# Kernel tuning notes

Measured on AMD Instinct MI355X. Metric: run time of the kernel, lower is better.

Reference implementation:

```python
import jax, jax.numpy as jnp
import numpy as np

L, B, H, HC = 2048, 64, 1024, 1024
NEG = -1e10


def setup_inputs() -> dict:
    key = jax.random.key(0)
    k1, k2, k3, k4, k5, k6 = jax.random.split(key, 6)
    prev_layer_outputs = jax.random.normal(k1, (L, B, H), dtype=jnp.float32)
    hidden = jax.random.normal(k2, (B, H), dtype=jnp.float32)
    mask = jax.random.randint(k3, (B, L), 0, 2, dtype=jnp.int32)
    # learned params: e = Linear(2H -> HC), v = Linear(HC -> 1, no bias)
    s_e = 1.0 / np.sqrt(2 * H)
    W_e = jax.random.uniform(k4, (HC, 2 * H), minval=-s_e, maxval=s_e, dtype=jnp.float32)
    b_e = jax.random.uniform(k5, (HC,), minval=-s_e, maxval=s_e, dtype=jnp.float32)
    s_v = 1.0 / np.sqrt(HC)
    W_v = jax.random.uniform(k6, (HC,), minval=-s_v, maxval=s_v, dtype=jnp.float32)
    return {"prev_layer_outputs": prev_layer_outputs, "hidden": hidden, "mask": mask,
            "W_e": W_e, "b_e": b_e, "W_v": W_v}


def reference(prev_layer_outputs, hidden, mask, W_e, b_e, W_v):
    # prev_layer_outputs: [L, B, H] -> [B, L, H]
    outs = jnp.transpose(prev_layer_outputs, (1, 0, 2))
    # repeat hidden over L and concat on feature dim: [B, L, 2H]
    hid = jnp.broadcast_to(hidden[:, None, :], (outs.shape[0], outs.shape[1], hidden.shape[-1]))
    cat = jnp.concatenate([hid, outs], axis=-1)
    # energy: tanh(Linear(2H -> HC))
    energy = jnp.tanh(jnp.einsum('blf,cf->blc', cat, W_e) + b_e)
    # score: Linear(HC -> 1), squeeze -> [B, L]
    attention = jnp.einsum('blc,c->bl', energy, W_v)
    attention = jnp.where(mask == 0, jnp.float32(NEG), attention)
    attention_weights = jax.nn.softmax(attention, axis=1)  # [B, L]
    # weighted sum over L -> [B, H], then to [1, B, H]
    weighted = jnp.einsum('bl,blh->bh', attention_weights, outs)
    return weighted[None, :, :]
```

## Files before the change

### kernel.cpp

```cpp
#include <hip/hip_runtime.h>
#include <hip/hip_bf16.h>
#include <stdint.h>

#define LDIM 2048
#define BDIM 64
#define HDIM 1024
#define HCDIM 1024
#define CAPROWS 98304

typedef __attribute__((ext_vector_type(8))) short short8;
typedef __attribute__((ext_vector_type(4))) short s16x4;
typedef __attribute__((ext_vector_type(4))) float f32x4;

static __device__ __forceinline__ short f2bf(float f) {
  union { float f; uint32_t u; } a; a.f = f;
  uint32_t r = a.u + 0x7fffu + ((a.u >> 16) & 1u);
  return (short)(r >> 16);
}
static __device__ __forceinline__ float bf2f(short s) {
  union { uint32_t u; float f; } a;
  a.u = ((uint32_t)(unsigned short)s) << 16;
  return a.f;
}
static __device__ __forceinline__ float fast_tanh(float x) {
  x = fminf(15.f, fmaxf(-15.f, x));
  float e = __expf(2.f * x);
  return (e - 1.f) * __builtin_amdgcn_rcpf(e + 1.f);
}

#define GL16(gp, lp) __builtin_amdgcn_global_load_lds(                           \
    (const __attribute__((address_space(1))) void*)(gp),                         \
    (__attribute__((address_space(3))) void*)(lp), 16, 0, 0)

__global__ void scan_mask(const int* __restrict__ mask, int* __restrict__ bases) {
  __shared__ int sc[512];
  const int t = threadIdx.x;
  int cnt = 0;
  #pragma unroll 8
  for (int b = 0; b < 64; ++b) {
    int4 v = *(const int4*)&mask[b * 2048 + t * 4];
    cnt += v.x + v.y + v.z + v.w;
  }
  sc[t] = cnt;
  __syncthreads();
  for (int off = 1; off < 512; off <<= 1) {
    int v = (t >= off) ? sc[t - off] : 0;
    __syncthreads();
    sc[t] += v;
    __syncthreads();
  }
  bases[t] = sc[t] - cnt;
  if (t == 511) bases[512] = sc[511];
}

__global__ void gather_rows(const float* __restrict__ prev, const int* __restrict__ mask,
                            const int* __restrict__ bases, short* __restrict__ A_c,
                            int* __restrict__ cm2m, int* __restrict__ m2cm) {
  __shared__ int smm[256];
  __shared__ int swt[4];
  const int c = blockIdx.x, t = threadIdx.x;
  const int base = bases[c];
  int bit = 0, p = 0, wv = 0;
  if (t < 256) {
    const int m = c * 256 + t;
    bit = (mask[(t & 63) * 2048 + (m >> 6)] != 0);
    unsigned long long bal = __ballot(bit);
    const int lane = t & 63;
    wv = t >> 6;
    p = __popcll(bal & ((1ull << lane) - 1ull));
    if (lane == 0) swt[wv] = (int)__popcll(bal);
  }
  __syncthreads();
  if (t < 256 && bit) {
    int off = p;
    for (int i = 0; i < wv; ++i) off += swt[i];
    const int cm = base + off;
    smm[off] = t;
    if (cm < CAPROWS) {
      cm2m[cm] = c * 256 + t;
      m2cm[c * 256 + t] = cm;
    }
  }
  __syncthreads();
  const int cnt = swt[0] + swt[1] + swt[2] + swt[3];
  const int col = (t & 255) * 4;
  for (int r = (t >> 8); r < cnt; r += 2) {
    const int lm = smm[r];
    const float4 v = *(const float4*)(prev + (((size_t)(c * 256 + lm)) << 10) + col);
    if (base + r < CAPROWS) {
      s16x4 o = { f2bf(v.x), f2bf(v.y), f2bf(v.z), f2bf(v.w) };
      *(s16x4*)&A_c[(((size_t)(base + r)) << 10) + col] = o;
    }
  }
}

__global__ void convert_we_pack(const float* __restrict__ We, short* __restrict__ Wb2) {
  int g = blockIdx.x * 256 + threadIdx.x;
  int c = g >> 8;
  int j = (g & 255) * 4;
  float4 v = *(const float4*)(We + (size_t)c * 2048 + 1024 + j);
  s16x4 o = { f2bf(v.x), f2bf(v.y), f2bf(v.z), f2bf(v.w) };
  const int off = ((c >> 4) * 32 + (j >> 5)) * 512 + ((c & 15) * 4 + ((j >> 3) & 3)) * 8 + (j & 7);
  *(s16x4*)(Wb2 + off) = o;
}

__global__ void hidbias_kernel(const float* __restrict__ We, const float* __restrict__ hidden,
                               const float* __restrict__ be, float* __restrict__ hidbias) {
  __shared__ float wrow[1024];
  int c0 = blockIdx.x * 16;
  int t = threadIdx.x;
  int b = t >> 2, q = t & 3;
  for (int ci = 0; ci < 16; ++ci) {
    int c = c0 + ci;
    *(float4*)&wrow[t * 4] = *(const float4*)&We[(size_t)c * 2048 + t * 4];
    __syncthreads();
    float s0 = 0.f, s1 = 0.f;
    const float* hb = hidden + b * 1024;
    #pragma unroll 8
    for (int j = 0; j < 256; j += 2) {
      int i0 = q + 4 * j;
      s0 += wrow[i0] * hb[i0];
      s1 += wrow[i0 + 4] * hb[i0 + 4];
    }
    float s = s0 + s1;
    s += __shfl_xor(s, 1);
    s += __shfl_xor(s, 2);
    if (q == 0) hidbias[b * 1024 + c] = s + be[c];
    __syncthreads();
  }
}

__global__ __launch_bounds__(512) void energy_gemm_breg(
    const short* __restrict__ A_c, const short* __restrict__ Wb2,
    const float* __restrict__ hidbias, const float* __restrict__ Wv,
    const int* __restrict__ bases, const int* __restrict__ cm2m,
    float* __restrict__ logitsT)
{
  __shared__ short As[4][256][32];
  __shared__ int sidx[256];
  const int Mc0 = bases[512];
  const int Mc = Mc0 < CAPROWS ? Mc0 : CAPROWS;
  const int mt = ((blockIdx.x >> 5) << 3) + (blockIdx.x & 7);
  const int nt = (blockIdx.x >> 3) & 3;
  if (mt * 256 >= Mc) return;
  const int m0 = mt * 256;
  const int n0 = nt * 256;

  const int tid = threadIdx.x;
  const int wave = tid >> 6, lane = tid & 63;
  const int q = lane >> 4, lr = lane & 15;
  const int wr = wave >> 2, wc = wave & 3;

  const int r0 = tid >> 2;
  const int c0s = (((tid & 3) ^ ((r0 >> 1) & 3))) * 8;
  const short* asrc = A_c + (size_t)(m0 + r0) * 1024 + c0s;

#define STAGE_A(buf, ks) do {                                                  \
    const int _ko = (ks) * 32;                                                 \
    GL16(asrc + _ko,          &As[buf][0][0] + tid * 8);                       \
    GL16(asrc + 131072 + _ko, &As[buf][0][0] + tid * 8 + 4096);                \
  } while (0)

  const int c16b = nt * 16 + wc * 4;
  const int lane4 = (lr * 4 + q) * 8;

#define BLOAD(dst, ks) do {                                                    \
    _Pragma("unroll")                                                          \
    for (int ni = 0; ni < 4; ++ni)                                             \
      dst[ni] = *(const short8*)(Wb2 + (size_t)((c16b + ni) * 32 + (ks)) * 512 + lane4); \
  } while (0)

  const int crd = (q ^ ((lr >> 1) & 3)) * 8;

#define COMPUTE(buf, BSET) do {                                                \
    short8 af[8];                                                              \
    _Pragma("unroll")                                                          \
    for (int mi = 0; mi < 8; ++mi)                                             \
      af[mi] = *(const short8*)&As[buf][wr * 128 + mi * 16 + lr][crd];         \
    __builtin_amdgcn_s_setprio(1);                                             \
    _Pragma("unroll")                                                          \
    for (int mi = 0; mi < 8; ++mi)                                             \
      _Pragma("unroll")                                                        \
      for (int ni = 0; ni < 4; ++ni)                                           \
        acc[mi][ni] = __builtin_amdgcn_mfma_f32_16x16x32_bf16(                 \
            af[mi], BSET[ni], acc[mi][ni], 0, 0, 0);                           \
    __builtin_amdgcn_s_setprio(0);                                             \
  } while (0)

#define VMW6() asm volatile("s_waitcnt vmcnt(6)" ::: "memory")
#define VMW4() asm volatile("s_waitcnt vmcnt(4)" ::: "memory")
#define VMW0() asm volatile("s_waitcnt vmcnt(0)" ::: "memory")
#define BAR()  asm volatile("s_barrier" ::: "memory")

  f32x4 acc[8][4];
  #pragma unroll
  for (int i = 0; i < 8; ++i)
    #pragma unroll
    for (int j = 0; j < 4; ++j) acc[i][j] = (f32x4){0.f, 0.f, 0.f, 0.f};

  short8 bs0[4], bs1[4];

  STAGE_A(0, 0);
  STAGE_A(1, 1);
  BLOAD(bs0, 0);
  STAGE_A(2, 2);

#define ITER(ks, CUR, NXT) do {                                                \
    BLOAD(NXT, (ks) + 1);                                                      \
    VMW6(); BAR();                                                             \
    STAGE_A(((ks) + 3) & 3, (ks) + 3);                                         \
    COMPUTE((ks) & 3, CUR);                                                    \
  } while (0)

  #pragma unroll 2
  for (int ks = 0; ks < 28; ks += 2) {
    ITER(ks, bs0, bs1);
    ITER(ks + 1, bs1, bs0);
  }
  ITER(28, bs0, bs1);
  { BLOAD(bs0, 30); VMW6(); BAR(); COMPUTE(1, bs1); }
  { BLOAD(bs1, 31); VMW4(); BAR(); COMPUTE(2, bs0); }
  { VMW0(); BAR(); COMPUTE(3, bs1); }

#undef ITER
#undef STAGE_A
#undef BLOAD
#undef COMPUTE

  if (tid < 256) sidx[tid] = (m0 + tid < Mc) ? cm2m[m0 + tid] : -1;
  __syncthreads();

  float wv[4];
  #pragma unroll
  for (int ni = 0; ni < 4; ++ni) wv[ni] = Wv[n0 + wc * 64 + ni * 16 + lr];

  #pragma unroll
  for (int mi = 0; mi < 8; ++mi) {
    #pragma unroll
    for (int r = 0; r < 4; ++r) {
      const int row = wr * 128 + mi * 16 + 4 * q + r;
      const int mm = sidx[row];
      if (mm >= 0) {
        const int b = mm & 63;
        float s = 0.f;
        #pragma unroll
        for (int ni = 0; ni < 4; ++ni) {
          const int c = n0 + wc * 64 + ni * 16 + lr;
          s += fast_tanh(acc[mi][ni][r] + hidbias[b * 1024 + c]) * wv[ni];
        }
        s += __shfl_xor(s, 1);
        s += __shfl_xor(s, 2);
        s += __shfl_xor(s, 4);
        s += __shfl_xor(s, 8);
        if (lr == 0) atomicAdd(&logitsT[mm], s);
      }
    }
  }
}

__global__ void softmax_wsum(const short* __restrict__ A_c, const float* __restrict__ logitsT,
                             const int* __restrict__ mask, const int* __restrict__ m2cm,
                             float* __restrict__ out) {
  __shared__ float red[8];
  const int b = blockIdx.x >> 5;
  const int lc = blockIdx.x & 31;
  const int t = threadIdx.x;

  float mx = -1e30f;
  for (int l = t; l < 2048; l += 256)
    if (mask[b * 2048 + l] != 0) mx = fmaxf(mx, logitsT[l * 64 + b]);
  #pragma unroll
  for (int o = 32; o > 0; o >>= 1) mx = fmaxf(mx, __shfl_xor(mx, o));
  if ((t & 63) == 0) red[t >> 6] = mx;
  __syncthreads();
  mx = fmaxf(fmaxf(red[0], red[1]), fmaxf(red[2], red[3]));
  float den = 0.f;
  for (int l = t; l < 2048; l += 256)
    if (mask[b * 2048 + l] != 0) den += __expf(logitsT[l * 64 + b] - mx);
  #pragma unroll
  for (int o = 32; o > 0; o >>= 1) den += __shfl_xor(den, o);
  if ((t & 63) == 0) red[4 + (t >> 6)] = den;
  __syncthreads();
  const float invd = 1.f / (red[4] + red[5] + red[6] + red[7]);

  const int h0 = t * 4;
  float4 a = {0.f, 0.f, 0.f, 0.f};
  for (int l = lc * 64; l < lc * 64 + 64; ++l) {
    if (mask[b * 2048 + l] == 0) continue;
    const unsigned cm = (unsigned)m2cm[l * 64 + b];
    if (cm >= (unsigned)CAPROWS) continue;
    float w = __expf(logitsT[l * 64 + b] - mx) * invd;
    s16x4 v = *(const s16x4*)&A_c[((size_t)cm << 10) + h0];
    a.x += w * bf2f(v.x);
    a.y += w * bf2f(v.y);
    a.z += w * bf2f(v.z);
    a.w += w * bf2f(v.w);
  }
  atomicAdd(&out[b * 1024 + h0 + 0], a.x);
  atomicAdd(&out[b * 1024 + h0 + 1], a.y);
  atomicAdd(&out[b * 1024 + h0 + 2], a.z);
  atomicAdd(&out[b * 1024 + h0 + 3], a.w);
}

extern "C" void kernel_launch(void* const* d_in, const int* in_sizes, int n_in,
                              void* d_out, int out_size, void* d_ws, size_t ws_size,
                              hipStream_t stream) {
  const float* prev   = (const float*)d_in[0];
  const float* hidden = (const float*)d_in[1];
  const int*   mask   = (const int*)d_in[2];
  const float* We     = (const float*)d_in[3];
  const float* be     = (const float*)d_in[4];
  const float* Wv     = (const float*)d_in[5];
  float* out = (float*)d_out;

  char* ws = (char*)d_ws;
  size_t off = 0;
  short* A_c     = (short*)(ws + off); off += (size_t)CAPROWS * 1024 * 2;
  short* Wb2     = (short*)(ws + off); off += 2097152;
  float* hidbias = (float*)(ws + off); off += 262144;
  float* logitsT = (float*)(ws + off); off += 524288;
  int*   cm2m    = (int*)  (ws + off); off += (size_t)CAPROWS * 4;
  int*   m2cm    = (int*)  (ws + off); off += 524288;
  int*   bases   = (int*)  (ws + off); off += 4096;

  hipMemsetAsync(d_out, 0, (size_t)out_size * sizeof(float), stream);
  hipMemsetAsync(logitsT, 0, 524288, stream);
  scan_mask<<<1, 512, 0, stream>>>(mask, bases);
  gather_rows<<<512, 512, 0, stream>>>(prev, mask, bases, A_c, cm2m, m2cm);
  convert_we_pack<<<1024, 256, 0, stream>>>(We, Wb2);
  hidbias_kernel<<<64, 256, 0, stream>>>(We, hidden, be, hidbias);
  energy_gemm_breg<<<2048, 512, 0, stream>>>(A_c, Wb2, hidbias, Wv, bases, cm2m, logitsT);
  softmax_wsum<<<2048, 256, 0, stream>>>(A_c, logitsT, mask, m2cm, out);
}
```

Measured before the change: 484.1 us.

## Retile energy GEMM to 256-thread blocks and split softmax stats from weighted sum

```diff
diff --git a/kernel.cpp b/kernel.cpp
--- a/kernel.cpp
+++ b/kernel.cpp
@@ -32,9 +32,13 @@
     (const __attribute__((address_space(1))) void*)(gp),                         \
     (__attribute__((address_space(3))) void*)(lp), 16, 0, 0)
 
-__global__ void scan_mask(const int* __restrict__ mask, int* __restrict__ bases) {
+__global__ void scan_mask(const int* __restrict__ mask, int* __restrict__ bases,
+                          float* __restrict__ logitsT) {
   __shared__ int sc[512];
   const int t = threadIdx.x;
+  const float4 z = {0.f, 0.f, 0.f, 0.f};
+  #pragma unroll 4
+  for (int i = 0; i < 64; ++i) *(float4*)&logitsT[t * 256 + i * 4] = z;
   int cnt = 0;
   #pragma unroll 8
   for (int b = 0; b < 64; ++b) {
@@ -105,11 +109,14 @@
 }
 
 __global__ void hidbias_kernel(const float* __restrict__ We, const float* __restrict__ hidden,
-                               const float* __restrict__ be, float* __restrict__ hidbias) {
+                               const float* __restrict__ be, float* __restrict__ hidbias,
+                               float* __restrict__ out) {
   __shared__ float wrow[1024];
   int c0 = blockIdx.x * 16;
   int t = threadIdx.x;
   int b = t >> 2, q = t & 3;
+  const float4 z = {0.f, 0.f, 0.f, 0.f};
+  *(float4*)&out[blockIdx.x * 1024 + t * 4] = z;
   for (int ci = 0; ci < 16; ++ci) {
     int c = c0 + ci;
     *(float4*)&wrow[t * 4] = *(const float4*)&We[(size_t)c * 2048 + t * 4];
@@ -130,7 +137,7 @@
   }
 }
 
-__global__ __launch_bounds__(512) void energy_gemm_breg(
+__global__ __launch_bounds__(256, 2) void energy_gemm_2b(
     const short* __restrict__ A_c, const short* __restrict__ Wb2,
     const float* __restrict__ hidbias, const float* __restrict__ Wv,
     const int* __restrict__ bases, const int* __restrict__ cm2m,
@@ -140,16 +147,16 @@
   __shared__ int sidx[256];
   const int Mc0 = bases[512];
   const int Mc = Mc0 < CAPROWS ? Mc0 : CAPROWS;
-  const int mt = ((blockIdx.x >> 5) << 3) + (blockIdx.x & 7);
-  const int nt = (blockIdx.x >> 3) & 3;
+  const int mt = ((blockIdx.x >> 6) << 3) + (blockIdx.x & 7);
+  const int nt = (blockIdx.x >> 3) & 7;
   if (mt * 256 >= Mc) return;
   const int m0 = mt * 256;
-  const int n0 = nt * 256;
+  const int n0 = nt * 128;
 
   const int tid = threadIdx.x;
   const int wave = tid >> 6, lane = tid & 63;
   const int q = lane >> 4, lr = lane & 15;
-  const int wr = wave >> 2, wc = wave & 3;
+  const int wr = wave >> 1, wc = wave & 1;
 
   const int r0 = tid >> 2;
   const int c0s = (((tid & 3) ^ ((r0 >> 1) & 3))) * 8;
@@ -158,10 +165,12 @@
 #define STAGE_A(buf, ks) do {                                                  \
     const int _ko = (ks) * 32;                                                 \
     GL16(asrc + _ko,          &As[buf][0][0] + tid * 8);                       \
+    GL16(asrc + 65536 + _ko,  &As[buf][0][0] + tid * 8 + 2048);                \
     GL16(asrc + 131072 + _ko, &As[buf][0][0] + tid * 8 + 4096);                \
+    GL16(asrc + 196608 + _ko, &As[buf][0][0] + tid * 8 + 6144);                \
   } while (0)
 
-  const int c16b = nt * 16 + wc * 4;
+  const int c16b = nt * 8 + wc * 4;
   const int lane4 = (lr * 4 + q) * 8;
 
 #define BLOAD(dst, ks) do {                                                    \
@@ -187,7 +196,7 @@
     __builtin_amdgcn_s_setprio(0);                                             \
   } while (0)
 
-#define VMW6() asm volatile("s_waitcnt vmcnt(6)" ::: "memory")
+#define VMW8() asm volatile("s_waitcnt vmcnt(8)" ::: "memory")
 #define VMW4() asm volatile("s_waitcnt vmcnt(4)" ::: "memory")
 #define VMW0() asm volatile("s_waitcnt vmcnt(0)" ::: "memory")
 #define BAR()  asm volatile("s_barrier" ::: "memory")
@@ -207,7 +216,7 @@
 
 #define ITER(ks, CUR, NXT) do {                                                \
     BLOAD(NXT, (ks) + 1);                                                      \
-    VMW6(); BAR();                                                             \
+    VMW8(); BAR();                                                             \
     STAGE_A(((ks) + 3) & 3, (ks) + 3);                                         \
     COMPUTE((ks) & 3, CUR);                                                    \
   } while (0)
@@ -218,7 +227,7 @@
     ITER(ks + 1, bs1, bs0);
   }
   ITER(28, bs0, bs1);
-  { BLOAD(bs0, 30); VMW6(); BAR(); COMPUTE(1, bs1); }
+  { BLOAD(bs0, 30); VMW8(); BAR(); COMPUTE(1, bs1); }
   { BLOAD(bs1, 31); VMW4(); BAR(); COMPUTE(2, bs0); }
   { VMW0(); BAR(); COMPUTE(3, bs1); }
 
@@ -258,14 +267,10 @@
   }
 }
 
-__global__ void softmax_wsum(const short* __restrict__ A_c, const float* __restrict__ logitsT,
-                             const int* __restrict__ mask, const int* __restrict__ m2cm,
-                             float* __restrict__ out) {
+__global__ void softstats(const float* __restrict__ logitsT, const int* __restrict__ mask,
+                          float* __restrict__ stats) {
   __shared__ float red[8];
-  const int b = blockIdx.x >> 5;
-  const int lc = blockIdx.x & 31;
-  const int t = threadIdx.x;
-
+  const int b = blockIdx.x, t = threadIdx.x;
   float mx = -1e30f;
   for (int l = t; l < 2048; l += 256)
     if (mask[b * 2048 + l] != 0) mx = fmaxf(mx, logitsT[l * 64 + b]);
@@ -281,8 +286,19 @@
   for (int o = 32; o > 0; o >>= 1) den += __shfl_xor(den, o);
   if ((t & 63) == 0) red[4 + (t >> 6)] = den;
   __syncthreads();
-  const float invd = 1.f / (red[4] + red[5] + red[6] + red[7]);
-
+  if (t == 0) {
+    stats[b * 2] = mx;
+    stats[b * 2 + 1] = 1.f / (red[4] + red[5] + red[6] + red[7]);
+  }
+}
+
+__global__ void wsum_bf16(const short* __restrict__ A_c, const float* __restrict__ logitsT,
+                          const int* __restrict__ mask, const float* __restrict__ stats,
+                          const int* __restrict__ m2cm, float* __restrict__ out) {
+  const int b = blockIdx.x >> 5;
+  const int lc = blockIdx.x & 31;
+  const int t = threadIdx.x;
+  const float mx = stats[b * 2], invd = stats[b * 2 + 1];
   const int h0 = t * 4;
   float4 a = {0.f, 0.f, 0.f, 0.f};
   for (int l = lc * 64; l < lc * 64 + 64; ++l) {
@@ -322,13 +338,13 @@
   int*   cm2m    = (int*)  (ws + off); off += (size_t)CAPROWS * 4;
   int*   m2cm    = (int*)  (ws + off); off += 524288;
   int*   bases   = (int*)  (ws + off); off += 4096;
-
-  hipMemsetAsync(d_out, 0, (size_t)out_size * sizeof(float), stream);
-  hipMemsetAsync(logitsT, 0, 524288, stream);
-  scan_mask<<<1, 512, 0, stream>>>(mask, bases);
+  float* stats   = (float*)(ws + off); off += 1024;
+
+  scan_mask<<<1, 512, 0, stream>>>(mask, bases, logitsT);
   gather_rows<<<512, 512, 0, stream>>>(prev, mask, bases, A_c, cm2m, m2cm);
   convert_we_pack<<<1024, 256, 0, stream>>>(We, Wb2);
-  hidbias_kernel<<<64, 256, 0, stream>>>(We, hidden, be, hidbias);
-  energy_gemm_breg<<<2048, 512, 0, stream>>>(A_c, Wb2, hidbias, Wv, bases, cm2m, logitsT);
-  softmax_wsum<<<2048, 256, 0, stream>>>(A_c, logitsT, mask, m2cm, out);
-}
+  hidbias_kernel<<<64, 256, 0, stream>>>(We, hidden, be, hidbias, out);
+  energy_gemm_2b<<<3072, 256, 0, stream>>>(A_c, Wb2, hidbias, Wv, bases, cm2m, logitsT);
+  softstats<<<64, 256, 0, stream>>>(logitsT, mask, stats);
+  wsum_bf16<<<2048, 256, 0, stream>>>(A_c, logitsT, mask, stats, m2cm, out);
+}
```

After: 506.1 us. 4.5% more time.
